# Kernel tuning notes

Measured on AMD Instinct MI355X. Metric: run time of the kernel, lower is better.

## Reference

```python
import jax, jax.numpy as jnp
import numpy as np

N = 50000      # nodes in frontier (degree-bucketed batch)
N_CH = 5       # max_output_degree / children per node
X = 256        # x_size
H = 256        # h_size


def setup_inputs() -> dict:
    key = jax.random.key(0)
    ks = jax.random.split(key, 8)
    s = 0.05  # param scale
    return {
        "x": jax.random.normal(ks[0], (N, X), dtype=jnp.float32),
        "x_mask": jnp.ones((N,), dtype=jnp.float32),
        "neighbour_h": jax.random.normal(ks[1], (N, N_CH, H), dtype=jnp.float32),
        "neighbour_c": jax.random.normal(ks[2], (N, N_CH, H), dtype=jnp.float32),
        "W_iou_in": jax.random.normal(ks[3], (X, 3 * H), dtype=jnp.float32) * s,
        "b_iou_in": jnp.zeros((3 * H,), dtype=jnp.float32),
        "W_f_in": jax.random.normal(ks[4], (X, H), dtype=jnp.float32) * s,
        "b_f_in": jnp.zeros((H,), dtype=jnp.float32),
        "W_aggr_iou": jax.random.normal(ks[5], (N_CH * H, 3 * H), dtype=jnp.float32) * s,
        "b_aggr_iou": jnp.zeros((3 * H,), dtype=jnp.float32),
        "W_aggr_f": jax.random.normal(ks[6], (N_CH * H, N_CH * H), dtype=jnp.float32) * s,
        "b_aggr_f": jnp.zeros((N_CH * H,), dtype=jnp.float32),
    }


def reference(x, x_mask, neighbour_h, neighbour_c,
              W_iou_in, b_iou_in, W_f_in, b_f_in,
              W_aggr_iou, b_aggr_iou, W_aggr_f, b_aggr_f):
    n_batch = neighbour_h.shape[0]
    n_ch = neighbour_h.shape[1]
    h_flat = neighbour_h.reshape(n_batch, n_ch * H)  # [N, n_ch*H]

    # forget gates (note: source adds f_input twice -- reproduced faithfully)
    f_input = (x @ W_f_in + b_f_in) * x_mask[:, None]          # [N, H]
    f_input = jnp.tile(f_input, (1, n_ch))                      # [N, n_ch*H]
    f_gate = h_flat @ W_aggr_f + b_aggr_f + f_input             # forget_module + f_input
    f_aggr = f_gate + f_input                                   # + f_input again (as in source)

    # iou aggregation over children
    iou_aggr = h_flat @ W_aggr_iou + b_aggr_iou                  # [N, 3H]

    f = jax.nn.sigmoid(f_aggr).reshape(n_batch, n_ch, H)
    c_aggr = jnp.sum(f * neighbour_c, axis=1)                    # [N, H]

    # apply_node_func
    iou = (x @ W_iou_in + b_iou_in) * x_mask[:, None] + iou_aggr
    i, o, u = jnp.split(iou, 3, axis=1)
    i, o, u = jax.nn.sigmoid(i), jax.nn.sigmoid(o), jnp.tanh(u)
    c = i * u + c_aggr
    h = o * jnp.tanh(c)
    return h, c
```

## Files before the change

### kernel.cpp

```cpp
#include <hip/hip_runtime.h>
#include <hip/hip_bf16.h>

typedef __bf16 bf16x8 __attribute__((ext_vector_type(8)));
typedef float floatx4 __attribute__((ext_vector_type(4)));

#define GLOBAL_AS __attribute__((address_space(1)))
#define LDS_AS __attribute__((address_space(3)))

constexpr int M_NODES = 50000;
constexpr int HSZ  = 256;
constexpr int KDIM = 1536;
constexpr int NDIM = 2048;
constexpr int BM = 128, BN = 128, BK = 32;
constexpr int MT = (M_NODES + BM - 1) / BM;
constexpr int NT = NDIM / BN;
constexpr size_t WCT_BYTES = (size_t)NDIM * KDIM * 2;
constexpr size_t A_BYTES   = (size_t)M_NODES * KDIM * 2;

__global__ __launch_bounds__(256) void prep_weights(
    const float* __restrict__ W_iou_in, const float* __restrict__ W_f_in,
    const float* __restrict__ W_aggr_iou, const float* __restrict__ W_aggr_f,
    __bf16* __restrict__ WcT)
{
  int idx = blockIdx.x * 256 + threadIdx.x;
  if (idx >= NDIM * KDIM) return;
  int n = idx / KDIM, k = idx - n * KDIM;
  int tb = n >> 7, rem = n & 127;
  int s = rem >> 4, tl = rem & 15;
  int t = tb * 16 + tl;
  float v;
  if (k < 256) {
    if (s < 5) v = 2.0f * W_f_in[k * 256 + t];
    else       v = W_iou_in[k * 768 + (s - 5) * 256 + t];
  } else {
    int kh = k - 256;
    if (s < 5) v = W_aggr_f[kh * 1280 + s * 256 + t];
    else       v = W_aggr_iou[kh * 768 + (s - 5) * 256 + t];
  }
  WcT[idx] = (__bf16)v;
}

__global__ __launch_bounds__(256) void prep_A(
    const float* __restrict__ x, const float* __restrict__ xmask,
    const float* __restrict__ nh, __bf16* __restrict__ Abf)
{
  int ci = blockIdx.x * 256 + threadIdx.x;
  if (ci >= M_NODES * (KDIM / 8)) return;
  int row = ci / (KDIM / 8);
  int kc  = ci - row * (KDIM / 8);
  const float* src;
  float sc;
  if (kc < 32) { src = x  + (size_t)row * 256  + kc * 8;        sc = xmask[row]; }
  else         { src = nh + (size_t)row * 1280 + (size_t)(kc - 32) * 8; sc = 1.0f; }
  float4 f0 = *(const float4*)src;
  float4 f1 = *(const float4*)(src + 4);
  bf16x8 v;
  v[0] = (__bf16)(f0.x * sc); v[1] = (__bf16)(f0.y * sc);
  v[2] = (__bf16)(f0.z * sc); v[3] = (__bf16)(f0.w * sc);
  v[4] = (__bf16)(f1.x * sc); v[5] = (__bf16)(f1.y * sc);
  v[6] = (__bf16)(f1.z * sc); v[7] = (__bf16)(f1.w * sc);
  *(bf16x8*)(Abf + (size_t)row * KDIM + kc * 8) = v;
}

__device__ __forceinline__ float sigm(float v) { return 1.0f / (1.0f + __expf(-v)); }
__device__ __forceinline__ float tanh_(float v) { return 2.0f / (1.0f + __expf(-2.0f * v)) - 1.0f; }

__global__ __launch_bounds__(256) void gemm_treelstm(
    const __bf16* __restrict__ Abf, const __bf16* __restrict__ WcT,
    const float* __restrict__ xmask, const float* __restrict__ nc,
    const float* __restrict__ b_iou, const float* __restrict__ b_f,
    const float* __restrict__ b_aiou, const float* __restrict__ b_af,
    float* __restrict__ out)
{
  __shared__ __bf16 ldsA[BM * BK];
  __shared__ __bf16 ldsB[BN * BK];

  const int tid = threadIdx.x;
  const int bn  = blockIdx.x;
  const int m0  = blockIdx.y * BM;

  const int lane = tid & 63;
  const int w    = tid >> 6;
  const int frow = lane & 15;
  const int kq   = lane >> 4;

  const int lrow = lane >> 2;
  const int cch  = (lane & 3) ^ ((lane >> 3) & 3);
  const int ar0  = m0 + w * 32 + lrow;
  const int ar1  = ar0 + 16;
  const __bf16* pA0 = Abf + (size_t)(ar0 < M_NODES ? ar0 : M_NODES - 1) * KDIM + cch * 8;
  const __bf16* pA1 = Abf + (size_t)(ar1 < M_NODES ? ar1 : M_NODES - 1) * KDIM + cch * 8;
  const __bf16* pB0 = WcT + (size_t)(bn * BN + w * 32 + lrow) * KDIM + cch * 8;
  const __bf16* pB1 = pB0 + (size_t)16 * KDIM;

  const int flane = ((kq ^ ((frow >> 1) & 3)) * 8);
  const int aoff0 = (w * 32 + frow) * BK + flane;
  const int aoff1 = aoff0 + 16 * BK;
  const int boff  = frow * BK + flane;

  floatx4 acc[2][8];
#pragma unroll
  for (int mt = 0; mt < 2; ++mt)
#pragma unroll
    for (int nt = 0; nt < 8; ++nt) acc[mt][nt] = (floatx4)(0.0f);

  for (int kt = 0; kt < KDIM / BK; ++kt) {
    __syncthreads();
    __builtin_amdgcn_global_load_lds((const GLOBAL_AS void*)pA0,
        (LDS_AS void*)((LDS_AS char*)(LDS_AS __bf16*)ldsA + (2 * w + 0) * 1024), 16, 0, 0);
    __builtin_amdgcn_global_load_lds((const GLOBAL_AS void*)pA1,
        (LDS_AS void*)((LDS_AS char*)(LDS_AS __bf16*)ldsA + (2 * w + 1) * 1024), 16, 0, 0);
    __builtin_amdgcn_global_load_lds((const GLOBAL_AS void*)pB0,
        (LDS_AS void*)((LDS_AS char*)(LDS_AS __bf16*)ldsB + (2 * w + 0) * 1024), 16, 0, 0);
    __builtin_amdgcn_global_load_lds((const GLOBAL_AS void*)pB1,
        (LDS_AS void*)((LDS_AS char*)(LDS_AS __bf16*)ldsB + (2 * w + 1) * 1024), 16, 0, 0);
    pA0 += BK; pA1 += BK; pB0 += BK; pB1 += BK;
    __syncthreads();

    bf16x8 a0 = *(const bf16x8*)&ldsA[aoff0];
    bf16x8 a1 = *(const bf16x8*)&ldsA[aoff1];
#pragma unroll
    for (int nt = 0; nt < 8; ++nt) {
      bf16x8 b = *(const bf16x8*)&ldsB[boff + nt * 512];
      acc[0][nt] = __builtin_amdgcn_mfma_f32_16x16x32_bf16(a0, b, acc[0][nt], 0, 0, 0);
      acc[1][nt] = __builtin_amdgcn_mfma_f32_16x16x32_bf16(a1, b, acc[1][nt], 0, 0, 0);
    }
  }

  const int t = bn * 16 + frow;
  float baf5[5];
#pragma unroll
  for (int s = 0; s < 5; ++s) baf5[s] = b_af[s * 256 + t];
  const float bf2 = 2.0f * b_f[t];
  float biou3[3], baiou3[3];
#pragma unroll
  for (int g = 0; g < 3; ++g) {
    biou3[g]  = b_iou[g * 256 + t];
    baiou3[g] = b_aiou[g * 256 + t];
  }

#pragma unroll
  for (int mt = 0; mt < 2; ++mt) {
#pragma unroll
    for (int j = 0; j < 4; ++j) {
      const int r = m0 + w * 32 + mt * 16 + kq * 4 + j;
      if (r >= M_NODES) continue;
      const float mk = xmask[r];
      float ca = 0.0f;
#pragma unroll
      for (int s = 0; s < 5; ++s) {
        const float fa = acc[mt][s][j] + baf5[s] + mk * bf2;
        ca += sigm(fa) * nc[((size_t)r * 5 + s) * 256 + t];
      }
      const float iv = sigm(acc[mt][5][j] + mk * biou3[0] + baiou3[0]);
      const float ov = sigm(acc[mt][6][j] + mk * biou3[1] + baiou3[1]);
      const float uv = tanh_(acc[mt][7][j] + mk * biou3[2] + baiou3[2]);
      const float c  = iv * uv + ca;
      const float h  = ov * tanh_(c);
      out[(size_t)r * HSZ + t] = h;
      out[(size_t)M_NODES * HSZ + (size_t)r * HSZ + t] = c;
    }
  }
}

constexpr int LDKF = 40;
__global__ __launch_bounds__(256) void fused_treelstm_fb(
    const float* __restrict__ x, const float* __restrict__ xmask,
    const float* __restrict__ nh, const float* __restrict__ nc,
    const float* __restrict__ b_iou, const float* __restrict__ b_f,
    const float* __restrict__ b_aiou, const float* __restrict__ b_af,
    const __bf16* __restrict__ WcT, float* __restrict__ out)
{
  __shared__ __bf16 ldsA[BM * LDKF];
  __shared__ __bf16 ldsB[BN * LDKF];
  const int tid = threadIdx.x;
  const int bn = blockIdx.x;
  const int m0 = blockIdx.y * BM;
  const int srow = tid >> 1;
  const int kc0  = tid & 1;
  const int arow_g = m0 + srow;
  const int arow_c = arow_g < M_NODES ? arow_g : M_NODES - 1;
  const float xm_stage = xmask[arow_c];
  const float* aptr_x = x  + (size_t)arow_c * 256;
  const float* aptr_h = nh + (size_t)arow_c * 1280 - 256;
  const __bf16* bptr  = WcT + (size_t)(bn * BN + srow) * KDIM;
  const int lane = tid & 63;
  const int w    = tid >> 6;
  const int frow = lane & 15;
  const int kq   = lane >> 4;
  floatx4 acc[2][8];
#pragma unroll
  for (int mt = 0; mt < 2; ++mt)
#pragma unroll
    for (int nt = 0; nt < 8; ++nt) acc[mt][nt] = (floatx4)(0.0f);
  for (int kt = 0; kt < KDIM / BK; ++kt) {
    const int k0 = kt * BK;
    __syncthreads();
#pragma unroll
    for (int i = 0; i < 2; ++i) {
      const int kl = (kc0 + 2 * i) * 8;
      const int kg = k0 + kl;
      const float* src = (kg < 256) ? (aptr_x + kg) : (aptr_h + kg);
      const float scale = (kg < 256) ? xm_stage : 1.0f;
      float4 f0 = *(const float4*)(src);
      float4 f1 = *(const float4*)(src + 4);
      bf16x8 va;
      va[0] = (__bf16)(f0.x * scale); va[1] = (__bf16)(f0.y * scale);
      va[2] = (__bf16)(f0.z * scale); va[3] = (__bf16)(f0.w * scale);
      va[4] = (__bf16)(f1.x * scale); va[5] = (__bf16)(f1.y * scale);
      va[6] = (__bf16)(f1.z * scale); va[7] = (__bf16)(f1.w * scale);
      *(bf16x8*)(&ldsA[srow * LDKF + kl]) = va;
      bf16x8 vb = *(const bf16x8*)(bptr + kg);
      *(bf16x8*)(&ldsB[srow * LDKF + kl]) = vb;
    }
    __syncthreads();
    bf16x8 a0 = *(const bf16x8*)&ldsA[(w * 32 + frow) * LDKF + kq * 8];
    bf16x8 a1 = *(const bf16x8*)&ldsA[(w * 32 + 16 + frow) * LDKF + kq * 8];
#pragma unroll
    for (int nt = 0; nt < 8; ++nt) {
      bf16x8 b = *(const bf16x8*)&ldsB[(nt * 16 + frow) * LDKF + kq * 8];
      acc[0][nt] = __builtin_amdgcn_mfma_f32_16x16x32_bf16(a0, b, acc[0][nt], 0, 0, 0);
      acc[1][nt] = __builtin_amdgcn_mfma_f32_16x16x32_bf16(a1, b, acc[1][nt], 0, 0, 0);
    }
  }
  const int t = bn * 16 + frow;
  float baf5[5];
#pragma unroll
  for (int s = 0; s < 5; ++s) baf5[s] = b_af[s * 256 + t];
  const float bf2 = 2.0f * b_f[t];
  float biou3[3], baiou3[3];
#pragma unroll
  for (int g = 0; g < 3; ++g) {
    biou3[g]  = b_iou[g * 256 + t];
    baiou3[g] = b_aiou[g * 256 + t];
  }
#pragma unroll
  for (int mt = 0; mt < 2; ++mt) {
#pragma unroll
    for (int j = 0; j < 4; ++j) {
      const int r = m0 + w * 32 + mt * 16 + kq * 4 + j;
      if (r >= M_NODES) continue;
      const float mk = xmask[r];
      float ca = 0.0f;
#pragma unroll
      for (int s = 0; s < 5; ++s) {
        const float fa = acc[mt][s][j] + baf5[s] + mk * bf2;
        ca += sigm(fa) * nc[((size_t)r * 5 + s) * 256 + t];
      }
      const float iv = sigm(acc[mt][5][j] + mk * biou3[0] + baiou3[0]);
      const float ov = sigm(acc[mt][6][j] + mk * biou3[1] + baiou3[1]);
      const float uv = tanh_(acc[mt][7][j] + mk * biou3[2] + baiou3[2]);
      const float c  = iv * uv + ca;
      const float h  = ov * tanh_(c);
      out[(size_t)r * HSZ + t] = h;
      out[(size_t)M_NODES * HSZ + (size_t)r * HSZ + t] = c;
    }
  }
}

extern "C" void kernel_launch(void* const* d_in, const int* in_sizes, int n_in,
                              void* d_out, int out_size, void* d_ws, size_t ws_size,
                              hipStream_t stream)
{
  const float* x      = (const float*)d_in[0];
  const float* xmask  = (const float*)d_in[1];
  const float* nh     = (const float*)d_in[2];
  const float* nc     = (const float*)d_in[3];
  const float* W_iou  = (const float*)d_in[4];
  const float* b_iou  = (const float*)d_in[5];
  const float* W_f    = (const float*)d_in[6];
  const float* b_f    = (const float*)d_in[7];
  const float* W_aiou = (const float*)d_in[8];
  const float* b_aiou = (const float*)d_in[9];
  const float* W_af   = (const float*)d_in[10];
  const float* b_af   = (const float*)d_in[11];
  __bf16* WcT = (__bf16*)d_ws;
  float* out  = (float*)d_out;

  prep_weights<<<(NDIM * KDIM + 255) / 256, 256, 0, stream>>>(W_iou, W_f, W_aiou, W_af, WcT);

  if (ws_size >= WCT_BYTES + A_BYTES) {
    __bf16* Abf = (__bf16*)((char*)d_ws + WCT_BYTES);
    prep_A<<<(M_NODES * (KDIM / 8) + 255) / 256, 256, 0, stream>>>(x, xmask, nh, Abf);
    gemm_treelstm<<<dim3(NT, MT), 256, 0, stream>>>(Abf, WcT, xmask, nc,
                                                    b_iou, b_f, b_aiou, b_af, out);
  } else {
    fused_treelstm_fb<<<dim3(NT, MT), 256, 0, stream>>>(x, xmask, nh, nc,
                                                        b_iou, b_f, b_aiou, b_af, WcT, out);
  }
}
```

Baseline: 1.115 ms.

## Enlarge GEMM tiles to 128x256x64 with XOR swizzle and XCD-aware block remap

Grows the block tile from 128x128x32 to 128x256x64 so each wave computes a 64x128 sub-tile with 4x8 MFMA fragments, which raises arithmetic intensity per LDS load. The LDS layout switches to an 8-chunk XOR swizzle to avoid bank conflicts. Block IDs are remapped over a 1D grid so that consecutive blocks spread across XCDs. Weight packing is adjusted to the new column interleave. The sigmoid and tanh helpers now use the hardware rcp instead of a divide. The cost is higher register pressure (128 accumulator floats per thread), which limits occupancy.

```diff
diff --git a/kernel.cpp b/kernel.cpp
--- a/kernel.cpp
+++ b/kernel.cpp
@@ -11,7 +11,7 @@
 constexpr int HSZ  = 256;
 constexpr int KDIM = 1536;
 constexpr int NDIM = 2048;
-constexpr int BM = 128, BN = 128, BK = 32;
+constexpr int BM = 128, BN = 256, BK = 64;
 constexpr int MT = (M_NODES + BM - 1) / BM;
 constexpr int NT = NDIM / BN;
 constexpr size_t WCT_BYTES = (size_t)NDIM * KDIM * 2;
@@ -25,9 +25,11 @@
   int idx = blockIdx.x * 256 + threadIdx.x;
   if (idx >= NDIM * KDIM) return;
   int n = idx / KDIM, k = idx - n * KDIM;
-  int tb = n >> 7, rem = n & 127;
-  int s = rem >> 4, tl = rem & 15;
-  int t = tb * 16 + tl;
+  int tb = n >> 8;
+  int u  = (n >> 7) & 1;
+  int s  = (n >> 4) & 7;
+  int tl = n & 15;
+  int t  = tb * 32 + u * 16 + tl;
   float v;
   if (k < 256) {
     if (s < 5) v = 2.0f * W_f_in[k * 256 + t];
@@ -62,168 +64,141 @@
   *(bf16x8*)(Abf + (size_t)row * KDIM + kc * 8) = v;
 }
 
-__device__ __forceinline__ float sigm(float v) { return 1.0f / (1.0f + __expf(-v)); }
-__device__ __forceinline__ float tanh_(float v) { return 2.0f / (1.0f + __expf(-2.0f * v)) - 1.0f; }
-
-__global__ __launch_bounds__(256) void gemm_treelstm(
+__device__ __forceinline__ float sigm(float v) {
+  return __builtin_amdgcn_rcpf(1.0f + __expf(-v));
+}
+__device__ __forceinline__ float tanh_(float v) {
+  return 2.0f * __builtin_amdgcn_rcpf(1.0f + __expf(-2.0f * v)) - 1.0f;
+}
+
+template <bool FROM_ABF>
+__global__ __launch_bounds__(256, 2) void gemm_treelstm2(
     const __bf16* __restrict__ Abf, const __bf16* __restrict__ WcT,
-    const float* __restrict__ xmask, const float* __restrict__ nc,
-    const float* __restrict__ b_iou, const float* __restrict__ b_f,
-    const float* __restrict__ b_aiou, const float* __restrict__ b_af,
-    float* __restrict__ out)
-{
-  __shared__ __bf16 ldsA[BM * BK];
-  __shared__ __bf16 ldsB[BN * BK];
-
-  const int tid = threadIdx.x;
-  const int bn  = blockIdx.x;
-  const int m0  = blockIdx.y * BM;
-
-  const int lane = tid & 63;
-  const int w    = tid >> 6;
-  const int frow = lane & 15;
-  const int kq   = lane >> 4;
-
-  const int lrow = lane >> 2;
-  const int cch  = (lane & 3) ^ ((lane >> 3) & 3);
-  const int ar0  = m0 + w * 32 + lrow;
-  const int ar1  = ar0 + 16;
-  const __bf16* pA0 = Abf + (size_t)(ar0 < M_NODES ? ar0 : M_NODES - 1) * KDIM + cch * 8;
-  const __bf16* pA1 = Abf + (size_t)(ar1 < M_NODES ? ar1 : M_NODES - 1) * KDIM + cch * 8;
-  const __bf16* pB0 = WcT + (size_t)(bn * BN + w * 32 + lrow) * KDIM + cch * 8;
-  const __bf16* pB1 = pB0 + (size_t)16 * KDIM;
-
-  const int flane = ((kq ^ ((frow >> 1) & 3)) * 8);
-  const int aoff0 = (w * 32 + frow) * BK + flane;
-  const int aoff1 = aoff0 + 16 * BK;
-  const int boff  = frow * BK + flane;
-
-  floatx4 acc[2][8];
-#pragma unroll
-  for (int mt = 0; mt < 2; ++mt)
-#pragma unroll
-    for (int nt = 0; nt < 8; ++nt) acc[mt][nt] = (floatx4)(0.0f);
-
-  for (int kt = 0; kt < KDIM / BK; ++kt) {
-    __syncthreads();
-    __builtin_amdgcn_global_load_lds((const GLOBAL_AS void*)pA0,
-        (LDS_AS void*)((LDS_AS char*)(LDS_AS __bf16*)ldsA + (2 * w + 0) * 1024), 16, 0, 0);
-    __builtin_amdgcn_global_load_lds((const GLOBAL_AS void*)pA1,
-        (LDS_AS void*)((LDS_AS char*)(LDS_AS __bf16*)ldsA + (2 * w + 1) * 1024), 16, 0, 0);
-    __builtin_amdgcn_global_load_lds((const GLOBAL_AS void*)pB0,
-        (LDS_AS void*)((LDS_AS char*)(LDS_AS __bf16*)ldsB + (2 * w + 0) * 1024), 16, 0, 0);
-    __builtin_amdgcn_global_load_lds((const GLOBAL_AS void*)pB1,
-        (LDS_AS void*)((LDS_AS char*)(LDS_AS __bf16*)ldsB + (2 * w + 1) * 1024), 16, 0, 0);
-    pA0 += BK; pA1 += BK; pB0 += BK; pB1 += BK;
-    __syncthreads();
-
-    bf16x8 a0 = *(const bf16x8*)&ldsA[aoff0];
-    bf16x8 a1 = *(const bf16x8*)&ldsA[aoff1];
-#pragma unroll
-    for (int nt = 0; nt < 8; ++nt) {
-      bf16x8 b = *(const bf16x8*)&ldsB[boff + nt * 512];
-      acc[0][nt] = __builtin_amdgcn_mfma_f32_16x16x32_bf16(a0, b, acc[0][nt], 0, 0, 0);
-      acc[1][nt] = __builtin_amdgcn_mfma_f32_16x16x32_bf16(a1, b, acc[1][nt], 0, 0, 0);
-    }
-  }
-
-  const int t = bn * 16 + frow;
-  float baf5[5];
-#pragma unroll
-  for (int s = 0; s < 5; ++s) baf5[s] = b_af[s * 256 + t];
-  const float bf2 = 2.0f * b_f[t];
-  float biou3[3], baiou3[3];
-#pragma unroll
-  for (int g = 0; g < 3; ++g) {
-    biou3[g]  = b_iou[g * 256 + t];
-    baiou3[g] = b_aiou[g * 256 + t];
-  }
-
-#pragma unroll
-  for (int mt = 0; mt < 2; ++mt) {
-#pragma unroll
-    for (int j = 0; j < 4; ++j) {
-      const int r = m0 + w * 32 + mt * 16 + kq * 4 + j;
-      if (r >= M_NODES) continue;
-      const float mk = xmask[r];
-      float ca = 0.0f;
-#pragma unroll
-      for (int s = 0; s < 5; ++s) {
-        const float fa = acc[mt][s][j] + baf5[s] + mk * bf2;
-        ca += sigm(fa) * nc[((size_t)r * 5 + s) * 256 + t];
-      }
-      const float iv = sigm(acc[mt][5][j] + mk * biou3[0] + baiou3[0]);
-      const float ov = sigm(acc[mt][6][j] + mk * biou3[1] + baiou3[1]);
-      const float uv = tanh_(acc[mt][7][j] + mk * biou3[2] + baiou3[2]);
-      const float c  = iv * uv + ca;
-      const float h  = ov * tanh_(c);
-      out[(size_t)r * HSZ + t] = h;
-      out[(size_t)M_NODES * HSZ + (size_t)r * HSZ + t] = c;
-    }
-  }
-}
-
-constexpr int LDKF = 40;
-__global__ __launch_bounds__(256) void fused_treelstm_fb(
     const float* __restrict__ x, const float* __restrict__ xmask,
     const float* __restrict__ nh, const float* __restrict__ nc,
     const float* __restrict__ b_iou, const float* __restrict__ b_f,
     const float* __restrict__ b_aiou, const float* __restrict__ b_af,
-    const __bf16* __restrict__ WcT, float* __restrict__ out)
-{
-  __shared__ __bf16 ldsA[BM * LDKF];
-  __shared__ __bf16 ldsB[BN * LDKF];
-  const int tid = threadIdx.x;
-  const int bn = blockIdx.x;
-  const int m0 = blockIdx.y * BM;
-  const int srow = tid >> 1;
-  const int kc0  = tid & 1;
-  const int arow_g = m0 + srow;
-  const int arow_c = arow_g < M_NODES ? arow_g : M_NODES - 1;
-  const float xm_stage = xmask[arow_c];
-  const float* aptr_x = x  + (size_t)arow_c * 256;
-  const float* aptr_h = nh + (size_t)arow_c * 1280 - 256;
-  const __bf16* bptr  = WcT + (size_t)(bn * BN + srow) * KDIM;
+    float* __restrict__ out)
+{
+  __shared__ __bf16 ldsA[BM * BK];
+  __shared__ __bf16 ldsB[BN * BK];
+
+  const int bid  = blockIdx.x;
+  const int wgid = (bid & 7) * (MT * NT / 8) + (bid >> 3);
+  const int bn   = wgid & 7;
+  const int m0   = (wgid >> 3) * BM;
+
+  const int tid  = threadIdx.x;
   const int lane = tid & 63;
   const int w    = tid >> 6;
-  const int frow = lane & 15;
-  const int kq   = lane >> 4;
-  floatx4 acc[2][8];
-#pragma unroll
-  for (int mt = 0; mt < 2; ++mt)
-#pragma unroll
-    for (int nt = 0; nt < 8; ++nt) acc[mt][nt] = (floatx4)(0.0f);
+  const int wr   = w >> 1, wc = w & 1;
+  const int frow = lane & 15, kq = lane >> 4;
+  const int l8   = lane >> 3, pch = lane & 7;
+
+  const __bf16* pA[4];
+  const __bf16* pB[8];
+  const float* xp[4]; const float* nhp[4]; float am[4]; int ac[4]; int arl[4];
+#pragma unroll
+  for (int j = 0; j < 4; ++j) {
+    const int rl = w * 32 + j * 8 + l8;
+    const int c  = pch ^ (rl & 7);
+    int gr = m0 + rl; if (gr >= M_NODES) gr = M_NODES - 1;
+    if constexpr (FROM_ABF) {
+      pA[j] = Abf + (size_t)gr * KDIM + c * 8;
+    } else {
+      arl[j] = rl; ac[j] = c;
+      xp[j]  = x  + (size_t)gr * 256;
+      nhp[j] = nh + (size_t)gr * 1280 - 256;
+      am[j]  = xmask[gr];
+    }
+  }
+#pragma unroll
+  for (int j = 0; j < 8; ++j) {
+    const int rl = w * 64 + j * 8 + l8;
+    const int c  = pch ^ (rl & 7);
+    pB[j] = WcT + (size_t)(bn * BN + rl) * KDIM + c * 8;
+  }
+
+  int aoff[4][2], boff[8][2];
+#pragma unroll
+  for (int mf = 0; mf < 4; ++mf) {
+    const int ra = wr * 64 + mf * 16 + frow;
+#pragma unroll
+    for (int ks = 0; ks < 2; ++ks)
+      aoff[mf][ks] = ra * BK + (((ks * 4 + kq) ^ (ra & 7)) * 8);
+  }
+#pragma unroll
+  for (int nf = 0; nf < 8; ++nf) {
+    const int rb = wc * 128 + nf * 16 + frow;
+#pragma unroll
+    for (int ks = 0; ks < 2; ++ks)
+      boff[nf][ks] = rb * BK + (((ks * 4 + kq) ^ (rb & 7)) * 8);
+  }
+
+  floatx4 acc[4][8];
+#pragma unroll
+  for (int i = 0; i < 4; ++i)
+#pragma unroll
+    for (int j = 0; j < 8; ++j) acc[i][j] = (floatx4)(0.0f);
+
   for (int kt = 0; kt < KDIM / BK; ++kt) {
-    const int k0 = kt * BK;
     __syncthreads();
-#pragma unroll
-    for (int i = 0; i < 2; ++i) {
-      const int kl = (kc0 + 2 * i) * 8;
-      const int kg = k0 + kl;
-      const float* src = (kg < 256) ? (aptr_x + kg) : (aptr_h + kg);
-      const float scale = (kg < 256) ? xm_stage : 1.0f;
-      float4 f0 = *(const float4*)(src);
-      float4 f1 = *(const float4*)(src + 4);
-      bf16x8 va;
-      va[0] = (__bf16)(f0.x * scale); va[1] = (__bf16)(f0.y * scale);
-      va[2] = (__bf16)(f0.z * scale); va[3] = (__bf16)(f0.w * scale);
-      va[4] = (__bf16)(f1.x * scale); va[5] = (__bf16)(f1.y * scale);
-      va[6] = (__bf16)(f1.z * scale); va[7] = (__bf16)(f1.w * scale);
-      *(bf16x8*)(&ldsA[srow * LDKF + kl]) = va;
-      bf16x8 vb = *(const bf16x8*)(bptr + kg);
-      *(bf16x8*)(&ldsB[srow * LDKF + kl]) = vb;
+    if constexpr (FROM_ABF) {
+#pragma unroll
+      for (int j = 0; j < 4; ++j) {
+        __builtin_amdgcn_global_load_lds((const GLOBAL_AS void*)pA[j],
+            (LDS_AS void*)((LDS_AS char*)(LDS_AS __bf16*)ldsA + (w * 32 + j * 8) * 128), 16, 0, 0);
+        pA[j] += BK;
+      }
+#pragma unroll
+      for (int j = 0; j < 8; ++j) {
+        __builtin_amdgcn_global_load_lds((const GLOBAL_AS void*)pB[j],
+            (LDS_AS void*)((LDS_AS char*)(LDS_AS __bf16*)ldsB + (w * 64 + j * 8) * 128), 16, 0, 0);
+        pB[j] += BK;
+      }
+    } else {
+      const int k0base = kt * BK;
+#pragma unroll
+      for (int j = 0; j < 4; ++j) {
+        const int k0 = k0base + ac[j] * 8;
+        const float* src = (k0 < 256) ? (xp[j] + k0) : (nhp[j] + k0);
+        const float sc   = (k0 < 256) ? am[j] : 1.0f;
+        float4 f0 = *(const float4*)src;
+        float4 f1 = *(const float4*)(src + 4);
+        bf16x8 v;
+        v[0] = (__bf16)(f0.x * sc); v[1] = (__bf16)(f0.y * sc);
+        v[2] = (__bf16)(f0.z * sc); v[3] = (__bf16)(f0.w * sc);
+        v[4] = (__bf16)(f1.x * sc); v[5] = (__bf16)(f1.y * sc);
+        v[6] = (__bf16)(f1.z * sc); v[7] = (__bf16)(f1.w * sc);
+        *(bf16x8*)&ldsA[arl[j] * BK + pch * 8] = v;
+      }
+#pragma unroll
+      for (int j = 0; j < 8; ++j) {
+        bf16x8 vb = *(const bf16x8*)pB[j];
+        *(bf16x8*)&ldsB[(w * 64 + j * 8 + l8) * BK + pch * 8] = vb;
+        pB[j] += BK;
+      }
     }
     __syncthreads();
-    bf16x8 a0 = *(const bf16x8*)&ldsA[(w * 32 + frow) * LDKF + kq * 8];
-    bf16x8 a1 = *(const bf16x8*)&ldsA[(w * 32 + 16 + frow) * LDKF + kq * 8];
-#pragma unroll
-    for (int nt = 0; nt < 8; ++nt) {
-      bf16x8 b = *(const bf16x8*)&ldsB[(nt * 16 + frow) * LDKF + kq * 8];
-      acc[0][nt] = __builtin_amdgcn_mfma_f32_16x16x32_bf16(a0, b, acc[0][nt], 0, 0, 0);
-      acc[1][nt] = __builtin_amdgcn_mfma_f32_16x16x32_bf16(a1, b, acc[1][nt], 0, 0, 0);
-    }
-  }
-  const int t = bn * 16 + frow;
+
+#pragma unroll
+    for (int ks = 0; ks < 2; ++ks) {
+      bf16x8 a0 = *(const bf16x8*)&ldsA[aoff[0][ks]];
+      bf16x8 a1 = *(const bf16x8*)&ldsA[aoff[1][ks]];
+      bf16x8 a2 = *(const bf16x8*)&ldsA[aoff[2][ks]];
+      bf16x8 a3 = *(const bf16x8*)&ldsA[aoff[3][ks]];
+#pragma unroll
+      for (int nf = 0; nf < 8; ++nf) {
+        bf16x8 b = *(const bf16x8*)&ldsB[boff[nf][ks]];
+        acc[0][nf] = __builtin_amdgcn_mfma_f32_16x16x32_bf16(a0, b, acc[0][nf], 0, 0, 0);
+        acc[1][nf] = __builtin_amdgcn_mfma_f32_16x16x32_bf16(a1, b, acc[1][nf], 0, 0, 0);
+        acc[2][nf] = __builtin_amdgcn_mfma_f32_16x16x32_bf16(a2, b, acc[2][nf], 0, 0, 0);
+        acc[3][nf] = __builtin_amdgcn_mfma_f32_16x16x32_bf16(a3, b, acc[3][nf], 0, 0, 0);
+      }
+    }
+  }
+
+  const int t = bn * 32 + wc * 16 + frow;
   float baf5[5];
 #pragma unroll
   for (int s = 0; s < 5; ++s) baf5[s] = b_af[s * 256 + t];
@@ -234,22 +209,23 @@
     biou3[g]  = b_iou[g * 256 + t];
     baiou3[g] = b_aiou[g * 256 + t];
   }
-#pragma unroll
-  for (int mt = 0; mt < 2; ++mt) {
+
+#pragma unroll
+  for (int mf = 0; mf < 4; ++mf) {
 #pragma unroll
     for (int j = 0; j < 4; ++j) {
-      const int r = m0 + w * 32 + mt * 16 + kq * 4 + j;
+      const int r = m0 + wr * 64 + mf * 16 + kq * 4 + j;
       if (r >= M_NODES) continue;
       const float mk = xmask[r];
       float ca = 0.0f;
 #pragma unroll
       for (int s = 0; s < 5; ++s) {
-        const float fa = acc[mt][s][j] + baf5[s] + mk * bf2;
+        const float fa = acc[mf][s][j] + baf5[s] + mk * bf2;
         ca += sigm(fa) * nc[((size_t)r * 5 + s) * 256 + t];
       }
-      const float iv = sigm(acc[mt][5][j] + mk * biou3[0] + baiou3[0]);
-      const float ov = sigm(acc[mt][6][j] + mk * biou3[1] + baiou3[1]);
-      const float uv = tanh_(acc[mt][7][j] + mk * biou3[2] + baiou3[2]);
+      const float iv = sigm(acc[mf][5][j] + mk * biou3[0] + baiou3[0]);
+      const float ov = sigm(acc[mf][6][j] + mk * biou3[1] + baiou3[1]);
+      const float uv = tanh_(acc[mf][7][j] + mk * biou3[2] + baiou3[2]);
       const float c  = iv * uv + ca;
       const float h  = ov * tanh_(c);
       out[(size_t)r * HSZ + t] = h;
@@ -282,10 +258,10 @@
   if (ws_size >= WCT_BYTES + A_BYTES) {
     __bf16* Abf = (__bf16*)((char*)d_ws + WCT_BYTES);
     prep_A<<<(M_NODES * (KDIM / 8) + 255) / 256, 256, 0, stream>>>(x, xmask, nh, Abf);
-    gemm_treelstm<<<dim3(NT, MT), 256, 0, stream>>>(Abf, WcT, xmask, nc,
-                                                    b_iou, b_f, b_aiou, b_af, out);
+    gemm_treelstm2<true><<<dim3(MT * NT), 256, 0, stream>>>(
+        Abf, WcT, x, xmask, nh, nc, b_iou, b_f, b_aiou, b_af, out);
   } else {
-    fused_treelstm_fb<<<dim3(NT, MT), 256, 0, stream>>>(x, xmask, nh, nc,
-                                                        b_iou, b_f, b_aiou, b_af, WcT, out);
-  }
-}
+    gemm_treelstm2<false><<<dim3(MT * NT), 256, 0, stream>>>(
+        nullptr, WcT, x, xmask, nh, nc, b_iou, b_f, b_aiou, b_af, out);
+  }
+}
```

Measured after the change: 920.8 us. -17.4%, faster.
